# Kernel optimization log

Hardware: AMD Instinct MI355X
Metric: run time of the kernel (lower is better)

Reference implementation:

```python
import jax, jax.numpy as jnp
import numpy as np

N = [80000, 70000, 50000]   # entities per type (flattened over the ragged batch)
F = [64, 128, 48]           # feature width per entity type
D = 512                     # d_model
B = 64                      # number of episodes in the ragged batch
EPS_IN = 1e-4               # InputNorm eps
EPS_LN = 1e-5               # LayerNorm eps
CLIP = 5.0                  # InputNorm cliprange


def setup_inputs() -> dict:
    key = jax.random.key(0)
    ks = jax.random.split(key, 3 * 7 + 2)
    inp = {}
    for i, (n, f) in enumerate(zip(N, F)):
        base = 7 * i
        inp[f"ent{i}"] = jax.random.normal(ks[base], (n, f), dtype=jnp.float32)
        inp[f"mean{i}"] = 0.1 * jax.random.normal(ks[base + 1], (f,), dtype=jnp.float32)
        inp[f"var{i}"] = jax.random.uniform(ks[base + 2], (f,), minval=0.5, maxval=1.5, dtype=jnp.float32)
        inp[f"W{i}"] = jax.random.normal(ks[base + 3], (f, D), dtype=jnp.float32) / np.sqrt(f)
        inp[f"b{i}"] = jnp.zeros((D,), dtype=jnp.float32)
        inp[f"gamma{i}"] = jnp.ones((D,), dtype=jnp.float32)
        inp[f"beta{i}"] = jnp.zeros((D,), dtype=jnp.float32)
    total = sum(N)
    # index_map: permutation reassembling per-type blocks into ragged episode order
    inp["index_map"] = jax.random.permutation(ks[-2], total).astype(jnp.int64)
    inp["batch_index"] = jnp.sort(jax.random.randint(ks[-1], (total,), 0, B)).astype(jnp.int64)
    return inp


def _embed(x, mean, var, W, b, gamma, beta):
    # InputNorm: normalize with running stats, clip outliers
    h = jnp.clip((x - mean) * jax.lax.rsqrt(var + EPS_IN), -CLIP, CLIP)
    # Linear + ReLU
    h = jnp.maximum(h @ W + b, 0.0)
    # LayerNorm
    mu = h.mean(-1, keepdims=True)
    v = ((h - mu) ** 2).mean(-1, keepdims=True)
    return gamma * (h - mu) * jax.lax.rsqrt(v + EPS_LN) + beta


def reference(ent0, mean0, var0, W0, b0, gamma0, beta0,
              ent1, mean1, var1, W1, b1, gamma1, beta1,
              ent2, mean2, var2, W2, b2, gamma2, beta2,
              index_map, batch_index):
    embeds = [
        _embed(ent0, mean0, var0, W0, b0, gamma0, beta0),
        _embed(ent1, mean1, var1, W1, b1, gamma1, beta1),
        _embed(ent2, mean2, var2, W2, b2, gamma2, beta2),
    ]
    x = jnp.concatenate(embeds, axis=0)                      # [sum(N), D]
    entity_type = jnp.concatenate(
        [jnp.full((n, 1), float(i), dtype=jnp.float32) for i, n in enumerate(N)], axis=0
    )
    # ragged reorder: gather-based reassembly into episode-major order
    x = x[index_map]
    entity_types = entity_type[index_map]
    tbatch_index = batch_index[index_map]
    return x, tbatch_index, entity_types
```

## Files before the change

### kernel.cpp

```cpp
#include <hip/hip_runtime.h>

#define DMODEL 512
#define EPS_IN 1e-4f
#define EPS_LN 1e-5f
#define CLIPV  5.0f

typedef float f32x4 __attribute__((ext_vector_type(4)));
typedef short s16x8 __attribute__((ext_vector_type(8)));

__device__ __forceinline__ unsigned short f2bf(float f) {
    union { float f; unsigned u; } v; v.f = f;
    unsigned r = v.u + 0x7fffu + ((v.u >> 16) & 1u);
    return (unsigned short)(r >> 16);
}

struct TypeParams {
    const float* x; const float* mean; const float* var;
    const unsigned short* Wt;
    const float* b; const float* gamma; const float* beta;
    int n;
    int offset;
    int nb;
};

__global__ __launch_bounds__(256) void setup_all(
    const int* __restrict__ index_map, const int* __restrict__ batch_index,
    int* __restrict__ inv, float* __restrict__ out_t, float* __restrict__ out_e,
    int total, int n0, int n01, int nbA,
    const float* __restrict__ W0, const float* __restrict__ W1, const float* __restrict__ W2,
    unsigned short* __restrict__ Wt0, unsigned short* __restrict__ Wt1, unsigned short* __restrict__ Wt2)
{
    if (blockIdx.x < (unsigned)nbA) {
        const int j = blockIdx.x * 256 + threadIdx.x;
        if (j >= total) return;
        const int r = index_map[j];
        inv[r] = j;
        out_t[j] = (float)batch_index[r];
        out_e[j] = (r < n0) ? 0.0f : ((r < n01) ? 1.0f : 2.0f);
    } else {
        int idx = (blockIdx.x - nbA) * 256 + threadIdx.x;
        const float* W; unsigned short* Wt; int K, Kp;
        if (idx < DMODEL * 64)              { W = W0; Wt = Wt0; K = 64;  Kp = 64; }
        else if (idx < DMODEL * (64 + 128)) { idx -= DMODEL * 64;  W = W1; Wt = Wt1; K = 128; Kp = 128; }
        else if (idx < DMODEL * 256)        { idx -= DMODEL * 192; W = W2; Wt = Wt2; K = 48;  Kp = 64; }
        else return;
        const int nn = idx / Kp, k = idx - nn * Kp;
        const float w = (k < K) ? W[(size_t)k * DMODEL + nn] : 0.0f;
        Wt[idx] = f2bf(w);
    }
}

template<int F, int KP>
__device__ __forceinline__ void embed_body(
    const TypeParams& p, int bid, const int* __restrict__ inv,
    float* __restrict__ out, char* lds)
{
    const int tid  = threadIdx.x;
    const int lane = tid & 63;
    const int wn   = tid >> 6;
    const int l15  = lane & 15;
    const int g    = lane >> 4;
    const int row0 = bid * 32;
    const int n    = p.n;

    constexpr int SEG = KP / 8;
#pragma unroll
    for (int idx = tid; idx < 32 * SEG; idx += 256) {
        const int r = idx / SEG;
        const int s = idx - r * SEG;
        const int c = s * 8;
        const int gr = row0 + r;
        s16x8 pk;
        if (gr < n && c < F) {
            const float4 x0 = *(const float4*)(p.x + (size_t)gr * F + c);
            const float4 x1 = *(const float4*)(p.x + (size_t)gr * F + c + 4);
            const float4 m0 = *(const float4*)(p.mean + c);
            const float4 m1 = *(const float4*)(p.mean + c + 4);
            const float4 v0 = *(const float4*)(p.var + c);
            const float4 v1 = *(const float4*)(p.var + c + 4);
            const float t[8] = {x0.x - m0.x, x0.y - m0.y, x0.z - m0.z, x0.w - m0.w,
                                x1.x - m1.x, x1.y - m1.y, x1.z - m1.z, x1.w - m1.w};
            const float iv[8] = {rsqrtf(v0.x + EPS_IN), rsqrtf(v0.y + EPS_IN),
                                 rsqrtf(v0.z + EPS_IN), rsqrtf(v0.w + EPS_IN),
                                 rsqrtf(v1.x + EPS_IN), rsqrtf(v1.y + EPS_IN),
                                 rsqrtf(v1.z + EPS_IN), rsqrtf(v1.w + EPS_IN)};
#pragma unroll
            for (int jj = 0; jj < 8; ++jj)
                pk[jj] = (short)f2bf(fminf(fmaxf(t[jj] * iv[jj], -CLIPV), CLIPV));
        } else {
#pragma unroll
            for (int jj = 0; jj < 8; ++jj) pk[jj] = 0;
        }
        int byte = r * (KP * 2) + s * 16;
        byte ^= (r & 7) << 4;
        *reinterpret_cast<s16x8*>(lds + byte) = pk;
    }
    __syncthreads();

    f32x4 acc[2][8];
#pragma unroll
    for (int m = 0; m < 2; ++m)
#pragma unroll
        for (int t = 0; t < 8; ++t) acc[m][t] = (f32x4)0.0f;

    const unsigned short* wtl = p.Wt + (size_t)(wn * 128 + l15) * KP + g * 8;

#pragma unroll
    for (int ks = 0; ks < KP / 32; ++ks) {
        const int kb = ks * 64 + g * 16;
        int a0b = l15 * (KP * 2) + kb;        a0b ^= (l15 & 7) << 4;
        int a1b = (l15 + 16) * (KP * 2) + kb; a1b ^= (l15 & 7) << 4;
        const s16x8 a0 = *reinterpret_cast<const s16x8*>(lds + a0b);
        const s16x8 a1 = *reinterpret_cast<const s16x8*>(lds + a1b);
#pragma unroll
        for (int t = 0; t < 8; ++t) {
            const s16x8 bf = *reinterpret_cast<const s16x8*>(wtl + (size_t)t * 16 * KP + ks * 32);
            acc[0][t] = __builtin_amdgcn_mfma_f32_16x16x32_bf16(a0, bf, acc[0][t], 0, 0, 0);
            acc[1][t] = __builtin_amdgcn_mfma_f32_16x16x32_bf16(a1, bf, acc[1][t], 0, 0, 0);
        }
    }

    float bv[8], gv[8], ev[8];
#pragma unroll
    for (int t = 0; t < 8; ++t) {
        const int col = wn * 128 + t * 16 + l15;
        bv[t] = p.b[col]; gv[t] = p.gamma[col]; ev[t] = p.beta[col];
    }

    {
        float ps[2][4] = {{0}}, pq[2][4] = {{0}};
#pragma unroll
        for (int m = 0; m < 2; ++m)
#pragma unroll
            for (int t = 0; t < 8; ++t)
#pragma unroll
                for (int j = 0; j < 4; ++j) {
                    const float v = fmaxf(acc[m][t][j] + bv[t], 0.0f);
                    ps[m][j] += v;
                    pq[m][j] = fmaf(v, v, pq[m][j]);
                }
#pragma unroll
        for (int off = 1; off < 16; off <<= 1)
#pragma unroll
            for (int m = 0; m < 2; ++m)
#pragma unroll
                for (int j = 0; j < 4; ++j) {
                    ps[m][j] += __shfl_xor(ps[m][j], off, 64);
                    pq[m][j] += __shfl_xor(pq[m][j], off, 64);
                }

        float2* red = reinterpret_cast<float2*>(lds + 32 * KP * 2);
        if (l15 == 0) {
#pragma unroll
            for (int m = 0; m < 2; ++m)
#pragma unroll
                for (int j = 0; j < 4; ++j) {
                    const int rl = m * 16 + 4 * g + j;
                    red[rl * 4 + wn] = make_float2(ps[m][j], pq[m][j]);
                }
        }
    }
    __syncthreads();

    const float2* red = reinterpret_cast<const float2*>(lds + 32 * KP * 2);

#pragma unroll
    for (int m = 0; m < 2; ++m)
#pragma unroll
        for (int j = 0; j < 4; ++j) {
            const int rl = m * 16 + 4 * g + j;
            const int rg = row0 + rl;
            if (rg >= n) continue;
            float s = 0.0f, q = 0.0f;
#pragma unroll
            for (int wq = 0; wq < 4; ++wq) { const float2 e = red[rl * 4 + wq]; s += e.x; q += e.y; }
            const float mu = s * (1.0f / DMODEL);
            const float vv = fmaxf(q * (1.0f / DMODEL) - mu * mu, 0.0f);
            const float sc = rsqrtf(vv + EPS_LN);
            const int orow = inv[p.offset + rg];
            float* op = out + (size_t)orow * DMODEL + wn * 128 + l15;
#pragma unroll
            for (int t = 0; t < 8; ++t) {
                const float v = fmaxf(acc[m][t][j] + bv[t], 0.0f);
                op[t * 16] = fmaf(gv[t] * sc, v - mu, ev[t]);
            }
        }
}

__global__ __launch_bounds__(256, 4) void embed_all(
    TypeParams p0, TypeParams p1, TypeParams p2,
    const int* __restrict__ inv, float* __restrict__ out)
{
    extern __shared__ char lds[];
    const int bid = blockIdx.x;
    if (bid < p0.nb)                embed_body<64, 64>  (p0, bid, inv, out, lds);
    else if (bid < p0.nb + p1.nb)   embed_body<128, 128>(p1, bid - p0.nb, inv, out, lds);
    else                            embed_body<48, 64>  (p2, bid - p0.nb - p1.nb, inv, out, lds);
}

extern "C" void kernel_launch(void* const* d_in, const int* in_sizes, int n_in,
                              void* d_out, int out_size, void* d_ws, size_t ws_size,
                              hipStream_t stream)
{
    const int F0 = 64, F1 = 128, F2 = 48;
    const int n0 = in_sizes[0]  / F0;
    const int n1 = in_sizes[7]  / F1;
    const int n2 = in_sizes[14] / F2;
    const int total = n0 + n1 + n2;

    float* out   = (float*)d_out;
    float* out_t = out + (size_t)total * DMODEL;
    float* out_e = out_t + total;

    int* inv = (int*)d_ws;
    unsigned short* Wt0 = (unsigned short*)((char*)d_ws + (((size_t)total * 4 + 255) & ~(size_t)255));
    unsigned short* Wt1 = Wt0 + DMODEL * 64;
    unsigned short* Wt2 = Wt1 + DMODEL * 128;

    const int* index_map   = (const int*)d_in[21];
    const int* batch_index = (const int*)d_in[22];

    const int nbA = (total + 255) / 256;
    const int nbB = (DMODEL * 256 + 255) / 256;
    setup_all<<<nbA + nbB, 256, 0, stream>>>(
        index_map, batch_index, inv, out_t, out_e, total, n0, n0 + n1, nbA,
        (const float*)d_in[3], (const float*)d_in[10], (const float*)d_in[17],
        Wt0, Wt1, Wt2);

    TypeParams p0{(const float*)d_in[0],  (const float*)d_in[1],  (const float*)d_in[2],
                  Wt0, (const float*)d_in[4],  (const float*)d_in[5],  (const float*)d_in[6],
                  n0, 0,       (n0 + 31) / 32};
    TypeParams p1{(const float*)d_in[7],  (const float*)d_in[8],  (const float*)d_in[9],
                  Wt1, (const float*)d_in[11], (const float*)d_in[12], (const float*)d_in[13],
                  n1, n0,      (n1 + 31) / 32};
    TypeParams p2{(const float*)d_in[14], (const float*)d_in[15], (const float*)d_in[16],
                  Wt2, (const float*)d_in[18], (const float*)d_in[19], (const float*)d_in[20],
                  n2, n0 + n1, (n2 + 31) / 32};

    const int nb = p0.nb + p1.nb + p2.nb;
    const int lds_size = 32 * 128 * 2 + 32 * 4 * sizeof(float2);
    embed_all<<<nb, 256, lds_size, stream>>>(p0, p1, p2, inv, out);
}
```

Baseline: 162.1 us.

## Gather rows in output order with a block-diagonal K=256 weight and folded bias

The kernel is restructured to walk output rows in episode order and read each input row through index_map, which removes the inverse-permutation pass and lets the 512-float output rows be written contiguously instead of scattered. All three types share one concatenated bf16 weight padded to K=256, with the per-type bias folded in through one-hot columns. Blocks grow to 64 rows and 512 threads. In exchange, every row does 256-wide MFMA work where it previously needed only 64 or 128, and the input loads become gathers.

```diff
diff --git a/kernel.cpp b/kernel.cpp
--- a/kernel.cpp
+++ b/kernel.cpp
@@ -1,6 +1,7 @@
 #include <hip/hip_runtime.h>
 
 #define DMODEL 512
+#define KPAD   256
 #define EPS_IN 1e-4f
 #define EPS_LN 1e-5f
 #define CLIPV  5.0f
@@ -14,84 +15,98 @@
     return (unsigned short)(r >> 16);
 }
 
-struct TypeParams {
-    const float* x; const float* mean; const float* var;
+__global__ __launch_bounds__(256) void build_wt(
+    const float* __restrict__ W0, const float* __restrict__ W1, const float* __restrict__ W2,
+    const float* __restrict__ b0, const float* __restrict__ b1, const float* __restrict__ b2,
+    unsigned short* __restrict__ Wt)
+{
+    const int idx = blockIdx.x * 256 + threadIdx.x;
+    const int col = idx >> 8, k = idx & 255;
+    float w;
+    if      (k <  64) w = W0[(size_t)k * DMODEL + col];
+    else if (k < 192) w = W1[(size_t)(k - 64) * DMODEL + col];
+    else if (k < 240) w = W2[(size_t)(k - 192) * DMODEL + col];
+    else if (k == 240) w = b0[col];
+    else if (k == 241) w = b1[col];
+    else if (k == 242) w = b2[col];
+    else w = 0.0f;
+    Wt[idx] = f2bf(w);
+}
+
+struct EmbedArgs {
+    const float *x0, *x1, *x2;
+    const float *mean0, *mean1, *mean2;
+    const float *var0, *var1, *var2;
+    const float *g0, *g1, *g2, *e0, *e1, *e2;
     const unsigned short* Wt;
-    const float* b; const float* gamma; const float* beta;
-    int n;
-    int offset;
-    int nb;
+    const int* index_map;
+    const int* batch_index;
+    float* out; float* out_t; float* out_e;
+    int n0, n01, total;
 };
 
-__global__ __launch_bounds__(256) void setup_all(
-    const int* __restrict__ index_map, const int* __restrict__ batch_index,
-    int* __restrict__ inv, float* __restrict__ out_t, float* __restrict__ out_e,
-    int total, int n0, int n01, int nbA,
-    const float* __restrict__ W0, const float* __restrict__ W1, const float* __restrict__ W2,
-    unsigned short* __restrict__ Wt0, unsigned short* __restrict__ Wt1, unsigned short* __restrict__ Wt2)
+__global__ __launch_bounds__(512, 4) void embed_all(EmbedArgs a)
 {
-    if (blockIdx.x < (unsigned)nbA) {
-        const int j = blockIdx.x * 256 + threadIdx.x;
-        if (j >= total) return;
-        const int r = index_map[j];
-        inv[r] = j;
-        out_t[j] = (float)batch_index[r];
-        out_e[j] = (r < n0) ? 0.0f : ((r < n01) ? 1.0f : 2.0f);
-    } else {
-        int idx = (blockIdx.x - nbA) * 256 + threadIdx.x;
-        const float* W; unsigned short* Wt; int K, Kp;
-        if (idx < DMODEL * 64)              { W = W0; Wt = Wt0; K = 64;  Kp = 64; }
-        else if (idx < DMODEL * (64 + 128)) { idx -= DMODEL * 64;  W = W1; Wt = Wt1; K = 128; Kp = 128; }
-        else if (idx < DMODEL * 256)        { idx -= DMODEL * 192; W = W2; Wt = Wt2; K = 48;  Kp = 64; }
-        else return;
-        const int nn = idx / Kp, k = idx - nn * Kp;
-        const float w = (k < K) ? W[(size_t)k * DMODEL + nn] : 0.0f;
-        Wt[idx] = f2bf(w);
-    }
-}
-
-template<int F, int KP>
-__device__ __forceinline__ void embed_body(
-    const TypeParams& p, int bid, const int* __restrict__ inv,
-    float* __restrict__ out, char* lds)
-{
+    __shared__ char lds[64 * KPAD * 2 + 64 * 4 * sizeof(float2) + 64 * sizeof(int)];
+    float2* red = reinterpret_cast<float2*>(lds + 64 * KPAD * 2);
+    int*   ityp = reinterpret_cast<int*>(lds + 64 * KPAD * 2 + 64 * 4 * sizeof(float2));
+
     const int tid  = threadIdx.x;
     const int lane = tid & 63;
-    const int wn   = tid >> 6;
+    const int w    = tid >> 6;
+    const int wm   = w >> 2;
+    const int wn   = w & 3;
     const int l15  = lane & 15;
     const int g    = lane >> 4;
-    const int row0 = bid * 32;
-    const int n    = p.n;
-
-    constexpr int SEG = KP / 8;
-#pragma unroll
-    for (int idx = tid; idx < 32 * SEG; idx += 256) {
-        const int r = idx / SEG;
-        const int s = idx - r * SEG;
-        const int c = s * 8;
-        const int gr = row0 + r;
+    const int row0 = blockIdx.x * 64;
+
+#pragma unroll
+    for (int it = 0; it < 4; ++it) {
+        const int idx = tid + it * 512;
+        const int r = idx >> 5, s = idx & 31;
+        const int j = row0 + r;
         s16x8 pk;
-        if (gr < n && c < F) {
-            const float4 x0 = *(const float4*)(p.x + (size_t)gr * F + c);
-            const float4 x1 = *(const float4*)(p.x + (size_t)gr * F + c + 4);
-            const float4 m0 = *(const float4*)(p.mean + c);
-            const float4 m1 = *(const float4*)(p.mean + c + 4);
-            const float4 v0 = *(const float4*)(p.var + c);
-            const float4 v1 = *(const float4*)(p.var + c + 4);
-            const float t[8] = {x0.x - m0.x, x0.y - m0.y, x0.z - m0.z, x0.w - m0.w,
-                                x1.x - m1.x, x1.y - m1.y, x1.z - m1.z, x1.w - m1.w};
-            const float iv[8] = {rsqrtf(v0.x + EPS_IN), rsqrtf(v0.y + EPS_IN),
-                                 rsqrtf(v0.z + EPS_IN), rsqrtf(v0.w + EPS_IN),
-                                 rsqrtf(v1.x + EPS_IN), rsqrtf(v1.y + EPS_IN),
-                                 rsqrtf(v1.z + EPS_IN), rsqrtf(v1.w + EPS_IN)};
-#pragma unroll
-            for (int jj = 0; jj < 8; ++jj)
-                pk[jj] = (short)f2bf(fminf(fmaxf(t[jj] * iv[jj], -CLIPV), CLIPV));
-        } else {
-#pragma unroll
-            for (int jj = 0; jj < 8; ++jj) pk[jj] = 0;
-        }
-        int byte = r * (KP * 2) + s * 16;
+#pragma unroll
+        for (int jj = 0; jj < 8; ++jj) pk[jj] = 0;
+
+        if (j < a.total) {
+            const int rg = a.index_map[j];
+            const float* xp; const float* mn; const float* vr;
+            int t, koff, F, rl;
+            if (rg < a.n0)       { t = 0; xp = a.x0; mn = a.mean0; vr = a.var0; koff = 0;   F = 64;  rl = rg; }
+            else if (rg < a.n01) { t = 1; xp = a.x1; mn = a.mean1; vr = a.var1; koff = 64;  F = 128; rl = rg - a.n0; }
+            else                 { t = 2; xp = a.x2; mn = a.mean2; vr = a.var2; koff = 192; F = 48;  rl = rg - a.n01; }
+
+            const int k0 = s * 8;
+            if (k0 >= koff && k0 < koff + F) {
+                const int c = k0 - koff;
+                const float4 xv0 = *(const float4*)(xp + (size_t)rl * F + c);
+                const float4 xv1 = *(const float4*)(xp + (size_t)rl * F + c + 4);
+                const float4 m0 = *(const float4*)(mn + c);
+                const float4 m1 = *(const float4*)(mn + c + 4);
+                const float4 v0 = *(const float4*)(vr + c);
+                const float4 v1 = *(const float4*)(vr + c + 4);
+                const float tv[8] = {xv0.x - m0.x, xv0.y - m0.y, xv0.z - m0.z, xv0.w - m0.w,
+                                     xv1.x - m1.x, xv1.y - m1.y, xv1.z - m1.z, xv1.w - m1.w};
+                const float iv[8] = {rsqrtf(v0.x + EPS_IN), rsqrtf(v0.y + EPS_IN),
+                                     rsqrtf(v0.z + EPS_IN), rsqrtf(v0.w + EPS_IN),
+                                     rsqrtf(v1.x + EPS_IN), rsqrtf(v1.y + EPS_IN),
+                                     rsqrtf(v1.z + EPS_IN), rsqrtf(v1.w + EPS_IN)};
+#pragma unroll
+                for (int jj = 0; jj < 8; ++jj)
+                    pk[jj] = (short)f2bf(fminf(fmaxf(tv[jj] * iv[jj], -CLIPV), CLIPV));
+            } else if (s == 30) {
+                pk[t] = (short)f2bf(1.0f);
+            }
+            if (s == 0) {
+                ityp[r] = t;
+                a.out_t[j] = (float)a.batch_index[rg];
+                a.out_e[j] = (float)t;
+            }
+        } else if (s == 0) {
+            ityp[r] = 0;
+        }
+        int byte = r * (KPAD * 2) + s * 16;
         byte ^= (r & 7) << 4;
         *reinterpret_cast<s16x8*>(lds + byte) = pk;
     }
@@ -103,30 +118,23 @@
 #pragma unroll
         for (int t = 0; t < 8; ++t) acc[m][t] = (f32x4)0.0f;
 
-    const unsigned short* wtl = p.Wt + (size_t)(wn * 128 + l15) * KP + g * 8;
-
-#pragma unroll
-    for (int ks = 0; ks < KP / 32; ++ks) {
-        const int kb = ks * 64 + g * 16;
-        int a0b = l15 * (KP * 2) + kb;        a0b ^= (l15 & 7) << 4;
-        int a1b = (l15 + 16) * (KP * 2) + kb; a1b ^= (l15 & 7) << 4;
+    const int arow = wm * 32 + l15;
+    const unsigned short* wtl = a.Wt + (size_t)(wn * 128 + l15) * KPAD + g * 8;
+
+#pragma unroll
+    for (int ks = 0; ks < KPAD / 32; ++ks) {
+        int a0b = arow * (KPAD * 2) + ks * 64 + g * 16;        a0b ^= (arow & 7) << 4;
+        int a1b = (arow + 16) * (KPAD * 2) + ks * 64 + g * 16; a1b ^= (arow & 7) << 4;
         const s16x8 a0 = *reinterpret_cast<const s16x8*>(lds + a0b);
         const s16x8 a1 = *reinterpret_cast<const s16x8*>(lds + a1b);
 #pragma unroll
         for (int t = 0; t < 8; ++t) {
-            const s16x8 bf = *reinterpret_cast<const s16x8*>(wtl + (size_t)t * 16 * KP + ks * 32);
+            const s16x8 bf = *reinterpret_cast<const s16x8*>(wtl + (size_t)t * 16 * KPAD + ks * 32);
             acc[0][t] = __builtin_amdgcn_mfma_f32_16x16x32_bf16(a0, bf, acc[0][t], 0, 0, 0);
             acc[1][t] = __builtin_amdgcn_mfma_f32_16x16x32_bf16(a1, bf, acc[1][t], 0, 0, 0);
         }
     }
 
-    float bv[8], gv[8], ev[8];
-#pragma unroll
-    for (int t = 0; t < 8; ++t) {
-        const int col = wn * 128 + t * 16 + l15;
-        bv[t] = p.b[col]; gv[t] = p.gamma[col]; ev[t] = p.beta[col];
-    }
-
     {
         float ps[2][4] = {{0}}, pq[2][4] = {{0}};
 #pragma unroll
@@ -134,68 +142,55 @@
 #pragma unroll
             for (int t = 0; t < 8; ++t)
 #pragma unroll
-                for (int j = 0; j < 4; ++j) {
-                    const float v = fmaxf(acc[m][t][j] + bv[t], 0.0f);
-                    ps[m][j] += v;
-                    pq[m][j] = fmaf(v, v, pq[m][j]);
+                for (int jj = 0; jj < 4; ++jj) {
+                    const float v = fmaxf(acc[m][t][jj], 0.0f);
+                    ps[m][jj] += v;
+                    pq[m][jj] = fmaf(v, v, pq[m][jj]);
                 }
 #pragma unroll
         for (int off = 1; off < 16; off <<= 1)
 #pragma unroll
             for (int m = 0; m < 2; ++m)
 #pragma unroll
-                for (int j = 0; j < 4; ++j) {
-                    ps[m][j] += __shfl_xor(ps[m][j], off, 64);
-                    pq[m][j] += __shfl_xor(pq[m][j], off, 64);
+                for (int jj = 0; jj < 4; ++jj) {
+                    ps[m][jj] += __shfl_xor(ps[m][jj], off, 64);
+                    pq[m][jj] += __shfl_xor(pq[m][jj], off, 64);
                 }
-
-        float2* red = reinterpret_cast<float2*>(lds + 32 * KP * 2);
         if (l15 == 0) {
 #pragma unroll
             for (int m = 0; m < 2; ++m)
 #pragma unroll
-                for (int j = 0; j < 4; ++j) {
-                    const int rl = m * 16 + 4 * g + j;
-                    red[rl * 4 + wn] = make_float2(ps[m][j], pq[m][j]);
+                for (int jj = 0; jj < 4; ++jj) {
+                    const int rl = wm * 32 + m * 16 + 4 * g + jj;
+                    red[rl * 4 + wn] = make_float2(ps[m][jj], pq[m][jj]);
                 }
         }
     }
     __syncthreads();
 
-    const float2* red = reinterpret_cast<const float2*>(lds + 32 * KP * 2);
-
 #pragma unroll
     for (int m = 0; m < 2; ++m)
 #pragma unroll
-        for (int j = 0; j < 4; ++j) {
-            const int rl = m * 16 + 4 * g + j;
-            const int rg = row0 + rl;
-            if (rg >= n) continue;
+        for (int jj = 0; jj < 4; ++jj) {
+            const int rl = wm * 32 + m * 16 + 4 * g + jj;
+            const int j = row0 + rl;
+            if (j >= a.total) continue;
             float s = 0.0f, q = 0.0f;
 #pragma unroll
             for (int wq = 0; wq < 4; ++wq) { const float2 e = red[rl * 4 + wq]; s += e.x; q += e.y; }
             const float mu = s * (1.0f / DMODEL);
             const float vv = fmaxf(q * (1.0f / DMODEL) - mu * mu, 0.0f);
             const float sc = rsqrtf(vv + EPS_LN);
-            const int orow = inv[p.offset + rg];
-            float* op = out + (size_t)orow * DMODEL + wn * 128 + l15;
-#pragma unroll
-            for (int t = 0; t < 8; ++t) {
-                const float v = fmaxf(acc[m][t][j] + bv[t], 0.0f);
-                op[t * 16] = fmaf(gv[t] * sc, v - mu, ev[t]);
+            const int t = ityp[rl];
+            const float* gp = (t == 0 ? a.g0 : (t == 1 ? a.g1 : a.g2)) + wn * 128 + l15;
+            const float* ep = (t == 0 ? a.e0 : (t == 1 ? a.e1 : a.e2)) + wn * 128 + l15;
+            float* op = a.out + (size_t)j * DMODEL + wn * 128 + l15;
+#pragma unroll
+            for (int tt = 0; tt < 8; ++tt) {
+                const float v = fmaxf(acc[m][tt][jj], 0.0f);
+                op[tt * 16] = fmaf(gp[tt * 16] * sc, v - mu, ep[tt * 16]);
             }
         }
-}
-
-__global__ __launch_bounds__(256, 4) void embed_all(
-    TypeParams p0, TypeParams p1, TypeParams p2,
-    const int* __restrict__ inv, float* __restrict__ out)
-{
-    extern __shared__ char lds[];
-    const int bid = blockIdx.x;
-    if (bid < p0.nb)                embed_body<64, 64>  (p0, bid, inv, out, lds);
-    else if (bid < p0.nb + p1.nb)   embed_body<128, 128>(p1, bid - p0.nb, inv, out, lds);
-    else                            embed_body<48, 64>  (p2, bid - p0.nb - p1.nb, inv, out, lds);
 }
 
 extern "C" void kernel_launch(void* const* d_in, const int* in_sizes, int n_in,
@@ -212,32 +207,25 @@
     float* out_t = out + (size_t)total * DMODEL;
     float* out_e = out_t + total;
 
-    int* inv = (int*)d_ws;
-    unsigned short* Wt0 = (unsigned short*)((char*)d_ws + (((size_t)total * 4 + 255) & ~(size_t)255));
-    unsigned short* Wt1 = Wt0 + DMODEL * 64;
-    unsigned short* Wt2 = Wt1 + DMODEL * 128;
-
-    const int* index_map   = (const int*)d_in[21];
-    const int* batch_index = (const int*)d_in[22];
-
-    const int nbA = (total + 255) / 256;
-    const int nbB = (DMODEL * 256 + 255) / 256;
-    setup_all<<<nbA + nbB, 256, 0, stream>>>(
-        index_map, batch_index, inv, out_t, out_e, total, n0, n0 + n1, nbA,
+    unsigned short* Wtc = (unsigned short*)d_ws;
+
+    build_wt<<<(DMODEL * KPAD) / 256, 256, 0, stream>>>(
         (const float*)d_in[3], (const float*)d_in[10], (const float*)d_in[17],
-        Wt0, Wt1, Wt2);
-
-    TypeParams p0{(const float*)d_in[0],  (const float*)d_in[1],  (const float*)d_in[2],
-                  Wt0, (const float*)d_in[4],  (const float*)d_in[5],  (const float*)d_in[6],
-                  n0, 0,       (n0 + 31) / 32};
-    TypeParams p1{(const float*)d_in[7],  (const float*)d_in[8],  (const float*)d_in[9],
-                  Wt1, (const float*)d_in[11], (const float*)d_in[12], (const float*)d_in[13],
-                  n1, n0,      (n1 + 31) / 32};
-    TypeParams p2{(const float*)d_in[14], (const float*)d_in[15], (const float*)d_in[16],
-                  Wt2, (const float*)d_in[18], (const float*)d_in[19], (const float*)d_in[20],
-                  n2, n0 + n1, (n2 + 31) / 32};
-
-    const int nb = p0.nb + p1.nb + p2.nb;
-    const int lds_size = 32 * 128 * 2 + 32 * 4 * sizeof(float2);
-    embed_all<<<nb, 256, lds_size, stream>>>(p0, p1, p2, inv, out);
-}
+        (const float*)d_in[4], (const float*)d_in[11], (const float*)d_in[18],
+        Wtc);
+
+    EmbedArgs a;
+    a.x0 = (const float*)d_in[0];  a.x1 = (const float*)d_in[7];  a.x2 = (const float*)d_in[14];
+    a.mean0 = (const float*)d_in[1];  a.mean1 = (const float*)d_in[8];   a.mean2 = (const float*)d_in[15];
+    a.var0  = (const float*)d_in[2];  a.var1  = (const float*)d_in[9];   a.var2  = (const float*)d_in[16];
+    a.g0 = (const float*)d_in[5];  a.g1 = (const float*)d_in[12]; a.g2 = (const float*)d_in[19];
+    a.e0 = (const float*)d_in[6];  a.e1 = (const float*)d_in[13]; a.e2 = (const float*)d_in[20];
+    a.Wt = Wtc;
+    a.index_map   = (const int*)d_in[21];
+    a.batch_index = (const int*)d_in[22];
+    a.out = out; a.out_t = out_t; a.out_e = out_e;
+    a.n0 = n0; a.n01 = n0 + n1; a.total = total;
+
+    const int nb = (total + 63) / 64;
+    embed_all<<<nb, 512, 0, stream>>>(a);
+}
```

Result: slower. 354.5 us (+118.7%).

## Use 8-wave blocks, precompute input-norm scale/shift, prefetch inverse indices

Applied to the files above, without the earlier changes.

The embed kernel now runs 512 threads per block, with each of the 8 waves computing 64 output columns instead of 128, which halves per-wave accumulator state and the MFMA chain. InputNorm is folded into a precomputed per-feature scale and shift, written once by an extra setup block, so each element needs one FMA instead of a subtract, rsqrt and multiply. The A tile in LDS is stored as a k-segment-major layout instead of a row-major XOR-swizzled one, and the output row indices from inv are loaded before the MFMA loop to hide their latency. The LayerNorm cross-wave reduction grows to 8 partials per row, and launch_bounds(512,4) may push register pressure up.

```diff
diff --git a/kernel.cpp b/kernel.cpp
--- a/kernel.cpp
+++ b/kernel.cpp
@@ -15,7 +15,8 @@
 }
 
 struct TypeParams {
-    const float* x; const float* mean; const float* var;
+    const float* x;
+    const float* ss;
     const unsigned short* Wt;
     const float* b; const float* gamma; const float* beta;
     int n;
@@ -28,8 +29,13 @@
     int* __restrict__ inv, float* __restrict__ out_t, float* __restrict__ out_e,
     int total, int n0, int n01, int nbA,
     const float* __restrict__ W0, const float* __restrict__ W1, const float* __restrict__ W2,
-    unsigned short* __restrict__ Wt0, unsigned short* __restrict__ Wt1, unsigned short* __restrict__ Wt2)
-{
+    unsigned short* __restrict__ Wt0, unsigned short* __restrict__ Wt1, unsigned short* __restrict__ Wt2,
+    const float* __restrict__ mean0, const float* __restrict__ var0,
+    const float* __restrict__ mean1, const float* __restrict__ var1,
+    const float* __restrict__ mean2, const float* __restrict__ var2,
+    float* __restrict__ ss0, float* __restrict__ ss1, float* __restrict__ ss2)
+{
+    const int nbB = (DMODEL * 256) / 256;
     if (blockIdx.x < (unsigned)nbA) {
         const int j = blockIdx.x * 256 + threadIdx.x;
         if (j >= total) return;
@@ -37,16 +43,20 @@
         inv[r] = j;
         out_t[j] = (float)batch_index[r];
         out_e[j] = (r < n0) ? 0.0f : ((r < n01) ? 1.0f : 2.0f);
-    } else {
+    } else if (blockIdx.x < (unsigned)(nbA + nbB)) {
         int idx = (blockIdx.x - nbA) * 256 + threadIdx.x;
         const float* W; unsigned short* Wt; int K, Kp;
         if (idx < DMODEL * 64)              { W = W0; Wt = Wt0; K = 64;  Kp = 64; }
         else if (idx < DMODEL * (64 + 128)) { idx -= DMODEL * 64;  W = W1; Wt = Wt1; K = 128; Kp = 128; }
-        else if (idx < DMODEL * 256)        { idx -= DMODEL * 192; W = W2; Wt = Wt2; K = 48;  Kp = 64; }
-        else return;
+        else                                { idx -= DMODEL * 192; W = W2; Wt = Wt2; K = 48;  Kp = 64; }
         const int nn = idx / Kp, k = idx - nn * Kp;
         const float w = (k < K) ? W[(size_t)k * DMODEL + nn] : 0.0f;
         Wt[idx] = f2bf(w);
+    } else {
+        const int c = threadIdx.x;
+        if (c < 64)  { const float s = rsqrtf(var0[c] + EPS_IN); ss0[c] = s; ss0[64 + c]  = -mean0[c] * s; }
+        if (c < 128) { const float s = rsqrtf(var1[c] + EPS_IN); ss1[c] = s; ss1[128 + c] = -mean1[c] * s; }
+        if (c < 48)  { const float s = rsqrtf(var2[c] + EPS_IN); ss2[c] = s; ss2[48 + c]  = -mean2[c] * s; }
     }
 }
 
@@ -62,68 +72,73 @@
     const int g    = lane >> 4;
     const int row0 = bid * 32;
     const int n    = p.n;
-
     constexpr int SEG = KP / 8;
-#pragma unroll
-    for (int idx = tid; idx < 32 * SEG; idx += 256) {
-        const int r = idx / SEG;
-        const int s = idx - r * SEG;
+    constexpr int NKS = KP / 32;
+
+    float2* red = reinterpret_cast<float2*>(lds + NKS * 2048);
+
+    if (tid < 32 * SEG) {
+        const int r = tid & 31;
+        const int s = tid >> 5;
+        const int gr = row0 + r;
         const int c = s * 8;
-        const int gr = row0 + r;
         s16x8 pk;
+#pragma unroll
+        for (int jj = 0; jj < 8; ++jj) pk[jj] = 0;
         if (gr < n && c < F) {
             const float4 x0 = *(const float4*)(p.x + (size_t)gr * F + c);
             const float4 x1 = *(const float4*)(p.x + (size_t)gr * F + c + 4);
-            const float4 m0 = *(const float4*)(p.mean + c);
-            const float4 m1 = *(const float4*)(p.mean + c + 4);
-            const float4 v0 = *(const float4*)(p.var + c);
-            const float4 v1 = *(const float4*)(p.var + c + 4);
-            const float t[8] = {x0.x - m0.x, x0.y - m0.y, x0.z - m0.z, x0.w - m0.w,
-                                x1.x - m1.x, x1.y - m1.y, x1.z - m1.z, x1.w - m1.w};
-            const float iv[8] = {rsqrtf(v0.x + EPS_IN), rsqrtf(v0.y + EPS_IN),
-                                 rsqrtf(v0.z + EPS_IN), rsqrtf(v0.w + EPS_IN),
-                                 rsqrtf(v1.x + EPS_IN), rsqrtf(v1.y + EPS_IN),
-                                 rsqrtf(v1.z + EPS_IN), rsqrtf(v1.w + EPS_IN)};
+            const float4 sc0 = *(const float4*)(p.ss + c);
+            const float4 sc1 = *(const float4*)(p.ss + c + 4);
+            const float4 sh0 = *(const float4*)(p.ss + F + c);
+            const float4 sh1 = *(const float4*)(p.ss + F + c + 4);
+            float t[8];
+            t[0] = fmaf(x0.x, sc0.x, sh0.x); t[1] = fmaf(x0.y, sc0.y, sh0.y);
+            t[2] = fmaf(x0.z, sc0.z, sh0.z); t[3] = fmaf(x0.w, sc0.w, sh0.w);
+            t[4] = fmaf(x1.x, sc1.x, sh1.x); t[5] = fmaf(x1.y, sc1.y, sh1.y);
+            t[6] = fmaf(x1.z, sc1.z, sh1.z); t[7] = fmaf(x1.w, sc1.w, sh1.w);
 #pragma unroll
             for (int jj = 0; jj < 8; ++jj)
-                pk[jj] = (short)f2bf(fminf(fmaxf(t[jj] * iv[jj], -CLIPV), CLIPV));
-        } else {
-#pragma unroll
-            for (int jj = 0; jj < 8; ++jj) pk[jj] = 0;
-        }
-        int byte = r * (KP * 2) + s * 16;
-        byte ^= (r & 7) << 4;
-        *reinterpret_cast<s16x8*>(lds + byte) = pk;
+                pk[jj] = (short)f2bf(fminf(fmaxf(t[jj], -CLIPV), CLIPV));
+        }
+        *reinterpret_cast<s16x8*>(lds + tid * 16) = pk;
     }
     __syncthreads();
 
-    f32x4 acc[2][8];
+    int orow[8];
 #pragma unroll
     for (int m = 0; m < 2; ++m)
 #pragma unroll
-        for (int t = 0; t < 8; ++t) acc[m][t] = (f32x4)0.0f;
-
-    const unsigned short* wtl = p.Wt + (size_t)(wn * 128 + l15) * KP + g * 8;
-
-#pragma unroll
-    for (int ks = 0; ks < KP / 32; ++ks) {
-        const int kb = ks * 64 + g * 16;
-        int a0b = l15 * (KP * 2) + kb;        a0b ^= (l15 & 7) << 4;
-        int a1b = (l15 + 16) * (KP * 2) + kb; a1b ^= (l15 & 7) << 4;
-        const s16x8 a0 = *reinterpret_cast<const s16x8*>(lds + a0b);
-        const s16x8 a1 = *reinterpret_cast<const s16x8*>(lds + a1b);
-#pragma unroll
-        for (int t = 0; t < 8; ++t) {
+        for (int j = 0; j < 4; ++j) {
+            const int rg = row0 + m * 16 + 4 * g + j;
+            orow[m * 4 + j] = (rg < n) ? inv[p.offset + rg] : -1;
+        }
+
+    f32x4 acc[2][4];
+#pragma unroll
+    for (int m = 0; m < 2; ++m)
+#pragma unroll
+        for (int t = 0; t < 4; ++t) acc[m][t] = (f32x4)0.0f;
+
+    const unsigned short* wtl = p.Wt + (size_t)(wn * 64 + l15) * KP + g * 8;
+
+#pragma unroll
+    for (int ks = 0; ks < NKS; ++ks) {
+        const int ab = ((ks * 4 + g) * 32 + l15) * 16;
+        const s16x8 a0 = *reinterpret_cast<const s16x8*>(lds + ab);
+        const s16x8 a1 = *reinterpret_cast<const s16x8*>(lds + ab + 256);
+#pragma unroll
+        for (int t = 0; t < 4; ++t) {
             const s16x8 bf = *reinterpret_cast<const s16x8*>(wtl + (size_t)t * 16 * KP + ks * 32);
             acc[0][t] = __builtin_amdgcn_mfma_f32_16x16x32_bf16(a0, bf, acc[0][t], 0, 0, 0);
             acc[1][t] = __builtin_amdgcn_mfma_f32_16x16x32_bf16(a1, bf, acc[1][t], 0, 0, 0);
         }
     }
 
-    float bv[8], gv[8], ev[8];
-#pragma unroll
-    for (int t = 0; t < 8; ++t) {
-        const int col = wn * 128 + t * 16 + l15;
+    float bv[4], gv[4], ev[4];
+#pragma unroll
+    for (int t = 0; t < 4; ++t) {
+        const int col = wn * 64 + t * 16 + l15;
         bv[t] = p.b[col]; gv[t] = p.gamma[col]; ev[t] = p.beta[col];
     }
 
@@ -132,7 +147,7 @@
 #pragma unroll
         for (int m = 0; m < 2; ++m)
 #pragma unroll
-            for (int t = 0; t < 8; ++t)
+            for (int t = 0; t < 4; ++t)
 #pragma unroll
                 for (int j = 0; j < 4; ++j) {
                     const float v = fmaxf(acc[m][t][j] + bv[t], 0.0f);
@@ -148,46 +163,41 @@
                     ps[m][j] += __shfl_xor(ps[m][j], off, 64);
                     pq[m][j] += __shfl_xor(pq[m][j], off, 64);
                 }
-
-        float2* red = reinterpret_cast<float2*>(lds + 32 * KP * 2);
         if (l15 == 0) {
 #pragma unroll
             for (int m = 0; m < 2; ++m)
 #pragma unroll
                 for (int j = 0; j < 4; ++j) {
                     const int rl = m * 16 + 4 * g + j;
-                    red[rl * 4 + wn] = make_float2(ps[m][j], pq[m][j]);
+                    red[rl * 8 + wn] = make_float2(ps[m][j], pq[m][j]);
                 }
         }
     }
     __syncthreads();
 
-    const float2* red = reinterpret_cast<const float2*>(lds + 32 * KP * 2);
-
 #pragma unroll
     for (int m = 0; m < 2; ++m)
 #pragma unroll
         for (int j = 0; j < 4; ++j) {
+            const int od = orow[m * 4 + j];
+            if (od < 0) continue;
             const int rl = m * 16 + 4 * g + j;
-            const int rg = row0 + rl;
-            if (rg >= n) continue;
             float s = 0.0f, q = 0.0f;
 #pragma unroll
-            for (int wq = 0; wq < 4; ++wq) { const float2 e = red[rl * 4 + wq]; s += e.x; q += e.y; }
+            for (int wq = 0; wq < 8; ++wq) { const float2 e = red[rl * 8 + wq]; s += e.x; q += e.y; }
             const float mu = s * (1.0f / DMODEL);
             const float vv = fmaxf(q * (1.0f / DMODEL) - mu * mu, 0.0f);
             const float sc = rsqrtf(vv + EPS_LN);
-            const int orow = inv[p.offset + rg];
-            float* op = out + (size_t)orow * DMODEL + wn * 128 + l15;
-#pragma unroll
-            for (int t = 0; t < 8; ++t) {
+            float* op = out + (size_t)od * DMODEL + wn * 64 + l15;
+#pragma unroll
+            for (int t = 0; t < 4; ++t) {
                 const float v = fmaxf(acc[m][t][j] + bv[t], 0.0f);
                 op[t * 16] = fmaf(gv[t] * sc, v - mu, ev[t]);
             }
         }
 }
 
-__global__ __launch_bounds__(256, 4) void embed_all(
+__global__ __launch_bounds__(512, 4) void embed_all(
     TypeParams p0, TypeParams p1, TypeParams p2,
     const int* __restrict__ inv, float* __restrict__ out)
 {
@@ -216,28 +226,35 @@
     unsigned short* Wt0 = (unsigned short*)((char*)d_ws + (((size_t)total * 4 + 255) & ~(size_t)255));
     unsigned short* Wt1 = Wt0 + DMODEL * 64;
     unsigned short* Wt2 = Wt1 + DMODEL * 128;
+    float* ss0 = (float*)(Wt2 + DMODEL * 64);
+    float* ss1 = ss0 + 128;
+    float* ss2 = ss1 + 256;
 
     const int* index_map   = (const int*)d_in[21];
     const int* batch_index = (const int*)d_in[22];
 
     const int nbA = (total + 255) / 256;
-    const int nbB = (DMODEL * 256 + 255) / 256;
-    setup_all<<<nbA + nbB, 256, 0, stream>>>(
+    const int nbB = (DMODEL * 256) / 256;
+    setup_all<<<nbA + nbB + 1, 256, 0, stream>>>(
         index_map, batch_index, inv, out_t, out_e, total, n0, n0 + n1, nbA,
         (const float*)d_in[3], (const float*)d_in[10], (const float*)d_in[17],
-        Wt0, Wt1, Wt2);
-
-    TypeParams p0{(const float*)d_in[0],  (const float*)d_in[1],  (const float*)d_in[2],
-                  Wt0, (const float*)d_in[4],  (const float*)d_in[5],  (const float*)d_in[6],
+        Wt0, Wt1, Wt2,
+        (const float*)d_in[1],  (const float*)d_in[2],
+        (const float*)d_in[8],  (const float*)d_in[9],
+        (const float*)d_in[15], (const float*)d_in[16],
+        ss0, ss1, ss2);
+
+    TypeParams p0{(const float*)d_in[0],  ss0, Wt0,
+                  (const float*)d_in[4],  (const float*)d_in[5],  (const float*)d_in[6],
                   n0, 0,       (n0 + 31) / 32};
-    TypeParams p1{(const float*)d_in[7],  (const float*)d_in[8],  (const float*)d_in[9],
-                  Wt1, (const float*)d_in[11], (const float*)d_in[12], (const float*)d_in[13],
+    TypeParams p1{(const float*)d_in[7],  ss1, Wt1,
+                  (const float*)d_in[11], (const float*)d_in[12], (const float*)d_in[13],
                   n1, n0,      (n1 + 31) / 32};
-    TypeParams p2{(const float*)d_in[14], (const float*)d_in[15], (const float*)d_in[16],
-                  Wt2, (const float*)d_in[18], (const float*)d_in[19], (const float*)d_in[20],
+    TypeParams p2{(const float*)d_in[14], ss2, Wt2,
+                  (const float*)d_in[18], (const float*)d_in[19], (const float*)d_in[20],
                   n2, n0 + n1, (n2 + 31) / 32};
 
     const int nb = p0.nb + p1.nb + p2.nb;
-    const int lds_size = 32 * 128 * 2 + 32 * 4 * sizeof(float2);
-    embed_all<<<nb, 256, lds_size, stream>>>(p0, p1, p2, inv, out);
-}
+    const int lds_size = 4 * 2048 + 32 * 8 * sizeof(float2);
+    embed_all<<<nb, 512, lds_size, stream>>>(p0, p1, p2, inv, out);
+}
```

After: 161.0 us. About the same (-0.7%).
